# Kernel optimization log

Hardware: AMD Instinct MI355X
Metric: run time of the kernel (lower is better)

## Reference

```python
import jax, jax.numpy as jnp
import numpy as np

H = 32      # num_attention_heads
HD = 64     # head_dim
MD = 64     # qk_mqa_dim (rope dim)
EPS = 1e-6
SCALING = (HD + MD) ** -0.5
NEG = -1e9


def rms_norm(x, w):
    var = jnp.mean(jnp.square(x), axis=-1, keepdims=True)
    return x * jax.lax.rsqrt(var + EPS) * w


def rotate_half(x):
    x1, x2 = jnp.split(x, 2, axis=-1)
    return jnp.concatenate([-x2, x1], axis=-1)


def apply_rope(x, cos, sin):
    return x * cos + rotate_half(x) * sin


def setup_inputs() -> dict:
    key = jax.random.key(0)
    ks = jax.random.split(key, 6)
    B, S, D = 1, 2048, 2048
    QR, KVR = 1024, 896
    hidden_states = jax.random.normal(ks[0], (B, S, D), jnp.float32)
    # real rotary tables for the MD-dim rope subspace
    inv_freq = 1.0 / (10000.0 ** (np.arange(0, MD, 2, dtype=np.float32) / MD))
    freqs = np.arange(S, dtype=np.float32)[:, None] * inv_freq[None, :]
    emb = np.concatenate([freqs, freqs], axis=-1)  # [S, MD]
    cos = jnp.asarray(np.cos(emb), jnp.float32)
    sin = jnp.asarray(np.sin(emb), jnp.float32)
    s = 0.02
    Wqa = jax.random.normal(ks[1], (QR, D), jnp.float32) * s
    q_ln_w = jnp.ones((QR,), jnp.float32)
    Wqb = jax.random.normal(ks[2], (H * (HD + MD), QR), jnp.float32) * s
    Wkva = jax.random.normal(ks[3], (KVR + MD, D), jnp.float32) * s
    kv_ln_w = jnp.ones((KVR,), jnp.float32)
    Wkvb = jax.random.normal(ks[4], (2 * H * HD, KVR), jnp.float32) * s
    Wo = jax.random.normal(ks[5], (D, H * HD), jnp.float32) * s
    return {"hidden_states": hidden_states, "cos": cos, "sin": sin,
            "Wqa": Wqa, "q_ln_w": q_ln_w, "Wqb": Wqb,
            "Wkva": Wkva, "kv_ln_w": kv_ln_w, "Wkvb": Wkvb, "Wo": Wo}


def reference(hidden_states, cos, sin, Wqa, q_ln_w, Wqb, Wkva, kv_ln_w, Wkvb, Wo):
    B, S, D = hidden_states.shape
    KVR = kv_ln_w.shape[0]
    # Q: LoRA down -> RMSNorm -> up (weights pre-absorbed with rope split)
    q = rms_norm(hidden_states @ Wqa.T, q_ln_w) @ Wqb.T      # [B,S,H*(HD+MD)]
    q = q.reshape(B, S, H, HD + MD).transpose(0, 2, 1, 3)     # [B,H,S,HD+MD]
    q_nope, q_rope = q[..., :HD], q[..., HD:]
    # KV: shared compressed latent + MQA rope key
    ckv = hidden_states @ Wkva.T                               # [B,S,KVR+MD]
    kv_nope, k_rope = ckv[..., :KVR], ckv[..., KVR:]
    kv_nope = rms_norm(kv_nope, kv_ln_w)
    q_rope = apply_rope(q_rope, cos[None, None], sin[None, None])
    k_rope = apply_rope(k_rope[:, None], cos[None, None], sin[None, None])  # [B,1,S,MD]
    # up-project latent to per-head K_nope and V (interleaved per head)
    kv = (kv_nope @ Wkvb.T).reshape(B, S, H, 2 * HD).transpose(0, 2, 1, 3)  # [B,H,S,2*HD]
    k_nope, value = kv[..., :HD], kv[..., HD:]
    key_states = jnp.concatenate(
        [k_nope, jnp.broadcast_to(k_rope, (B, H, S, MD))], axis=-1)  # repeat_kv of rope part
    query_states = jnp.concatenate([q_nope, q_rope], axis=-1)        # [B,H,S,HD+MD]
    # causal SDPA with scaling = (head_dim + qk_mqa_dim)^-0.5
    scores = jnp.einsum('bhqd,bhkd->bhqk', query_states, key_states) * SCALING
    causal = jnp.tril(jnp.ones((S, S), bool))
    scores = jnp.where(causal[None, None], scores, NEG)
    probs = jax.nn.softmax(scores, axis=-1)
    out = jnp.einsum('bhqk,bhkd->bhqd', probs, value)                # [B,H,S,HD]
    out = out.transpose(0, 2, 1, 3).reshape(B, S, H * HD)
    return out @ Wo.T
```

## Files before the change

kernel.cpp:

```cpp
#include <hip/hip_runtime.h>
#include <stdint.h>

typedef unsigned short u16;
typedef __attribute__((ext_vector_type(4))) float f32x4;
typedef __attribute__((ext_vector_type(4))) unsigned short u16x4;
typedef __attribute__((ext_vector_type(8))) unsigned short u16x8;
typedef __attribute__((ext_vector_type(8))) short s16x8;
typedef __attribute__((ext_vector_type(4))) short s16x4;
typedef __attribute__((ext_vector_type(2))) unsigned int u32x2;

#define DEVI static __device__ __forceinline__

#define VMCNT(n) asm volatile("s_waitcnt vmcnt(" #n ")" ::: "memory")
#define SBAR() __builtin_amdgcn_s_barrier()
#define SCHED0() __builtin_amdgcn_sched_barrier(0)

DEVI u16 f2b(float f) {
  union { float f; unsigned u; } v; v.f = f;
  unsigned r = v.u + 0x7fffu + ((v.u >> 16) & 1u);
  return (u16)(r >> 16);
}
DEVI float b2f(u16 b) {
  union { unsigned u; float f; } v; v.u = ((unsigned)b) << 16;
  return v.f;
}

DEVI void gload_lds16(const void* gptr, void* lptr) {
  typedef const __attribute__((address_space(1))) unsigned gq;
  typedef __attribute__((address_space(3))) unsigned lq;
  __builtin_amdgcn_global_load_lds((gq*)(uintptr_t)gptr,
                                   (lq*)(uint32_t)(uintptr_t)lptr, 16, 0, 0);
}

DEVI unsigned cvtpk(float a, float b) {
  unsigned d;
  asm("v_cvt_pk_bf16_f32 %0, %1, %2" : "=v"(d) : "v"(a), "v"(b));
  return d;
}
DEVI f32x4 mfma16(s16x4 a, s16x4 b, f32x4 c) {
  f32x4 d;
  asm("v_mfma_f32_16x16x16_bf16 %0, %1, %2, %3" : "=v"(d) : "v"(a), "v"(b), "v"(c));
  return d;
}
DEVI float exp2a(float x) {
  float d;
  asm("v_exp_f32 %0, %1" : "=v"(d) : "v"(x));
  return d;
}

__global__ __launch_bounds__(256) void cvt_all(
    const float* __restrict__ X, const float* __restrict__ Wqa,
    const float* __restrict__ Wkva, const float* __restrict__ Wqb,
    const float* __restrict__ Wkvb, const float* __restrict__ Wo,
    u16* __restrict__ Xb, u16* __restrict__ W1, u16* __restrict__ Wqbb,
    u16* __restrict__ Wkvbb, u16* __restrict__ Wob) {
  int i = blockIdx.x * 256 + threadIdx.x;
  const int stride = gridDim.x * 256;
  for (; i < 5079040; i += stride) {
    const float* s; u16* d; int j;
    if (i < 1572864) {
      if (i < 1048576) { s = X; d = Xb; j = i; }
      else             { s = Wqa; d = W1; j = i - 1048576; }
    } else if (i < 3112960) {
      if (i < 2064384) { s = Wkva; d = W1 + 1024 * 2048; j = i - 1572864; }
      else             { s = Wqb; d = Wqbb; j = i - 2064384; }
    } else {
      if (i < 4030464) { s = Wkvb; d = Wkvbb; j = i - 3112960; }
      else             { s = Wo; d = Wob; j = i - 4030464; }
    }
    f32x4 v = *(const f32x4*)(s + (size_t)j * 4);
    u16x4 o;
    o[0] = f2b(v[0]); o[1] = f2b(v[1]); o[2] = f2b(v[2]); o[3] = f2b(v[3]);
    *(u16x4*)(d + (size_t)j * 4) = o;
  }
}

#define GEMM_STAGE(AP, BP, KK, k0, buf)                                        \
  {                                                                            \
    _Pragma("unroll") for (int p = 0; p < 4; ++p) {                            \
      const int c = tid + p * 256;                                             \
      const int row = c >> 3, j = c & 7;                                       \
      gload_lds16(AP + (size_t)(m0 + row) * (KK) + (k0) + ((j ^ (row & 7)) * 8), \
                  &As[buf][c * 8]);                                            \
    }                                                                          \
    _Pragma("unroll") for (int p = 0; p < 4; ++p) {                            \
      const int c = tid + p * 256;                                             \
      const int row = c >> 3, j = c & 7;                                       \
      gload_lds16(BP + (size_t)(n0 + row) * (KK) + (k0) + ((j ^ (row & 7)) * 8), \
                  &Bs[buf][c * 8]);                                            \
    }                                                                          \
  }

#define GEMM_COMPUTE(cur)                                                      \
  _Pragma("unroll") for (int kk = 0; kk < 64; kk += 32) {                      \
    s16x8 af[4], bfr[4];                                                       \
    _Pragma("unroll") for (int i = 0; i < 4; ++i) {                            \
      const int rA = wm * 64 + i * 16 + c15;                                   \
      af[i] = *(const s16x8*)((const char*)&As[cur][0] + rA * 128 +            \
                              (((kk + g * 8) * 2) ^ ((rA & 7) << 4)));         \
    }                                                                          \
    _Pragma("unroll") for (int i = 0; i < 4; ++i) {                            \
      const int rB = wn * 64 + i * 16 + c15;                                   \
      bfr[i] = *(const s16x8*)((const char*)&Bs[cur][0] + rB * 128 +           \
                               (((kk + g * 8) * 2) ^ ((rB & 7) << 4)));        \
    }                                                                          \
    _Pragma("unroll") for (int i = 0; i < 4; ++i)                              \
      _Pragma("unroll") for (int j = 0; j < 4; ++j)                            \
        acc[i][j] = __builtin_amdgcn_mfma_f32_16x16x32_bf16(af[i], bfr[j],     \
                                                            acc[i][j], 0, 0, 0); \
  }

#define GEMM_PROLOG                                                            \
  const int tid = threadIdx.x;                                                 \
  const int lane = tid & 63, w = tid >> 6;                                     \
  const int wm = w >> 1, wn = w & 1;                                           \
  const int c15 = lane & 15, g = lane >> 4;                                    \
  const int m0 = blockIdx.y * 128, n0 = blockIdx.x * 128;                      \
  f32x4 acc[4][4] = {};

#define GEMM_LOOP(AP, BP, KK)                                                  \
  GEMM_STAGE(AP, BP, KK, 0, 0);                                                \
  const int nk = (KK) >> 6;                                                    \
  for (int kt = 0; kt < nk; ++kt) {                                            \
    const int cur = kt & 1;                                                    \
    if (kt + 1 < nk) {                                                         \
      GEMM_STAGE(AP, BP, KK, (kt + 1) << 6, cur ^ 1);                          \
      VMCNT(8);                                                                \
    } else {                                                                   \
      VMCNT(0);                                                                \
    }                                                                          \
    SBAR(); SCHED0();                                                          \
    GEMM_COMPUTE(cur);                                                         \
    SBAR(); SCHED0();                                                          \
  }

#define GEMM_LOOP3(AP, BP, KK)                                                 \
  GEMM_STAGE(AP, BP, KK, 0, 0);                                                \
  GEMM_STAGE(AP, BP, KK, 64, 1);                                               \
  const int nk = (KK) >> 6;                                                    \
  int bufc = 0;                                                                \
  for (int kt = 0; kt < nk; ++kt) {                                            \
    const int nxt = (bufc + 2 >= 3) ? bufc - 1 : bufc + 2;                     \
    if (kt + 2 < nk) {                                                         \
      GEMM_STAGE(AP, BP, KK, (kt + 2) << 6, nxt);                              \
      VMCNT(16);                                                               \
    } else if (kt + 1 < nk) {                                                  \
      VMCNT(8);                                                                \
    } else {                                                                   \
      VMCNT(0);                                                                \
    }                                                                          \
    SBAR(); SCHED0();                                                          \
    GEMM_COMPUTE(bufc);                                                        \
    SBAR(); SCHED0();                                                          \
    bufc = (bufc + 1 == 3) ? 0 : bufc + 1;                                     \
  }

template <int OUT_BF16>
__global__ __launch_bounds__(256) void gemm_out(const u16* __restrict__ A,
                                                const u16* __restrict__ B,
                                                void* __restrict__ Cv,
                                                int M, int N, int K) {
  __shared__ __align__(16) u16 As[3][128 * 64];
  __shared__ __align__(16) u16 Bs[3][128 * 64];
  GEMM_PROLOG
  GEMM_LOOP3(A, B, K)
#pragma unroll
  for (int i = 0; i < 4; ++i)
#pragma unroll
    for (int j = 0; j < 4; ++j) {
      const int mr = m0 + wm * 64 + i * 16 + g * 4;
      const int nc = n0 + wn * 64 + j * 16 + c15;
#pragma unroll
      for (int r = 0; r < 4; ++r) {
        if (OUT_BF16)
          ((u16*)Cv)[(size_t)(mr + r) * N + nc] = f2b(acc[i][j][r]);
        else
          ((float*)Cv)[(size_t)(mr + r) * N + nc] = acc[i][j][r];
      }
    }
}

__global__ __launch_bounds__(256) void gemm2_fused(
    const u16* __restrict__ qn, const u16* __restrict__ Wqbb,
    const u16* __restrict__ kvn, const u16* __restrict__ Wkvbb,
    u16* __restrict__ qraw, char* __restrict__ KbB, char* __restrict__ VtB) {
  __shared__ __align__(16) u16 As[2][128 * 64];
  __shared__ __align__(16) u16 Bs[2][128 * 64];
  const int z = blockIdx.z;
  const u16* A = z ? kvn : qn;
  const u16* B = z ? Wkvbb : Wqbb;
  const int K = z ? 896 : 1024;
  GEMM_PROLOG
  GEMM_LOOP(A, B, K)

  if (z == 0) {
#pragma unroll
    for (int i = 0; i < 4; ++i)
#pragma unroll
      for (int j = 0; j < 4; ++j) {
        const int mr = m0 + wm * 64 + i * 16 + g * 4;
        const int nc = n0 + wn * 64 + j * 16 + c15;
#pragma unroll
        for (int r = 0; r < 4; ++r)
          qraw[(size_t)(mr + r) * 4096 + nc] = f2b(acc[i][j][r]);
      }
  } else {
    const int h = n0 >> 7;
#pragma unroll
    for (int i = 0; i < 4; ++i)
#pragma unroll
      for (int j = 0; j < 4; ++j) {
        const int mr = m0 + wm * 64 + i * 16 + g * 4;
        if (wn == 0) {
          const int d = j * 16 + c15;
#pragma unroll
          for (int r = 0; r < 4; ++r) {
            const int s = mr + r;
            *(u16*)(KbB + ((size_t)(h * 2048 + s) << 8) +
                    ((2 * d) ^ ((s & 7) << 4))) = f2b(acc[i][j][r]);
          }
        } else {
          const int d = j * 16 + c15;
          u16x4 o;
#pragma unroll
          for (int r = 0; r < 4; ++r) o[r] = f2b(acc[i][j][r]);
          *(u16x4*)(VtB + ((size_t)(h * 64 + d) << 12) +
                    ((2 * mr) ^ ((d & 7) << 4))) = o;
        }
      }
  }
}

DEVI float block_sum(float v, float* sbuf, int tid) {
#pragma unroll
  for (int o = 32; o; o >>= 1) v += __shfl_xor(v, o, 64);
  __syncthreads();
  if ((tid & 63) == 0) sbuf[tid >> 6] = v;
  __syncthreads();
  return sbuf[0] + sbuf[1] + sbuf[2] + sbuf[3];
}

__global__ __launch_bounds__(256) void norm_rope(const u16* __restrict__ C1b,
    const float* __restrict__ qw, const float* __restrict__ kw,
    const float* __restrict__ cosb, const float* __restrict__ sinb,
    u16* __restrict__ qn, u16* __restrict__ kvn, char* __restrict__ KbB) {
  __shared__ float sbuf[4];
  __shared__ __align__(16) u16 rv[64];
  const int s = blockIdx.x, tid = threadIdx.x;
  const u16* row = C1b + (size_t)s * 2048;

  u16x4 qv4 = *(const u16x4*)(row + tid * 4);
  float q0 = b2f(qv4[0]), q1 = b2f(qv4[1]), q2 = b2f(qv4[2]), q3 = b2f(qv4[3]);
  float ss = q0*q0 + q1*q1 + q2*q2 + q3*q3;
  ss = block_sum(ss, sbuf, tid);
  const float scale = rsqrtf(ss * (1.f / 1024.f) + 1e-6f);
  {
    f32x4 wv = *(const f32x4*)(qw + tid * 4);
    u16x4 o;
    o[0] = f2b(q0 * scale * wv[0]); o[1] = f2b(q1 * scale * wv[1]);
    o[2] = f2b(q2 * scale * wv[2]); o[3] = f2b(q3 * scale * wv[3]);
    *(u16x4*)(qn + (size_t)s * 1024 + tid * 4) = o;
  }

  float ss2 = 0.f;
  float k0 = 0, k1 = 0, k2 = 0, k3 = 0;
  if (tid < 224) {
    u16x4 kv4 = *(const u16x4*)(row + 1024 + tid * 4);
    k0 = b2f(kv4[0]); k1 = b2f(kv4[1]); k2 = b2f(kv4[2]); k3 = b2f(kv4[3]);
    ss2 = k0*k0 + k1*k1 + k2*k2 + k3*k3;
  }
  ss2 = block_sum(ss2, sbuf, tid);
  const float sc2 = rsqrtf(ss2 * (1.f / 896.f) + 1e-6f);
  if (tid < 224) {
    f32x4 wv = *(const f32x4*)(kw + tid * 4);
    u16x4 o;
    o[0] = f2b(k0 * sc2 * wv[0]); o[1] = f2b(k1 * sc2 * wv[1]);
    o[2] = f2b(k2 * sc2 * wv[2]); o[3] = f2b(k3 * sc2 * wv[3]);
    *(u16x4*)(kvn + (size_t)s * 896 + tid * 4) = o;
  }

  if (tid < 64) {
    const int d = tid;
    const float x = b2f(row[1920 + d]);
    const float part = b2f(row[1920 + (d < 32 ? d + 32 : d - 32)]);
    const float cv = cosb[s * 64 + d], sv = sinb[s * 64 + d];
    rv[d] = f2b(d < 32 ? (x * cv - part * sv) : (x * cv + part * sv));
  }
  __syncthreads();
  {
    const int h = tid >> 3, c8 = tid & 7;
    const u16x8 v = *(const u16x8*)&rv[c8 * 8];
    *(u16x8*)(KbB + ((size_t)(h * 2048 + s) << 8) +
              ((128 + c8 * 16) ^ ((s & 7) << 4))) = v;
  }
}

__global__ __launch_bounds__(256) void attn_fwd(
    const u16* __restrict__ Qb, const u16* __restrict__ Kb,
    const u16* __restrict__ Vt, const float* __restrict__ cosb,
    const float* __restrict__ sinb, u16* __restrict__ attn) {
  __shared__ __align__(16) u16 Klds[2][64 * 128];
  __shared__ __align__(16) u16 Vlds[2][64 * 64];
  const int tid = threadIdx.x;
  const int lane = tid & 63, w = tid >> 6;
  const int c15 = lane & 15, g = lane >> 4;
  const int orig = blockIdx.x;
  const int xcd = orig & 7, l = orig >> 3;
  const int h = xcd * 4 + (l & 3);
  const int x = l >> 2;
  const int qb = (x < 8) ? (15 - x) : (x - 8);
  const int wmin = qb * 128 + w * 32;
  const int wmax = wmin + 31;
  const char* KbHB = (const char*)Kb + ((size_t)h << 19);
  const char* VtHB = (const char*)Vt + ((size_t)h << 18);
  const float SC2 = 0.12753860478587782f;

  s16x8 qf[2][4];
#pragma unroll
  for (int qa = 0; qa < 2; ++qa) {
    const int qrow = wmin + qa * 16 + c15;
    const u16* qp = Qb + (size_t)qrow * 4096 + h * 128;
    u16x8 x0 = *(const u16x8*)(qp + g * 8);
    u16x8 x1 = *(const u16x8*)(qp + 32 + g * 8);
    u16x8 x2 = *(const u16x8*)(qp + 64 + g * 8);
    u16x8 x3 = *(const u16x8*)(qp + 96 + g * 8);
    const float* cb = cosb + (size_t)qrow * 64 + g * 8;
    const float* sb = sinb + (size_t)qrow * 64 + g * 8;
#pragma unroll
    for (int i = 0; i < 8; ++i) {
      qf[qa][0][i] = (short)f2b(b2f(x0[i]) * SC2);
      qf[qa][1][i] = (short)f2b(b2f(x1[i]) * SC2);
      const float f2 = b2f(x2[i]), f3 = b2f(x3[i]);
      qf[qa][2][i] = (short)f2b((f2 * cb[i] - f3 * sb[i]) * SC2);
      qf[qa][3][i] = (short)f2b((f3 * cb[32 + i] + f2 * sb[32 + i]) * SC2);
    }
  }

  const int nt = 2 * qb + 2;
  auto STAGE = [&](int t, int buf) {
    const int kv0 = t << 6;
#pragma unroll
    for (int p = 0; p < 4; ++p) {
      const int c = tid + p * 256;
      gload_lds16(KbHB + ((size_t)(kv0 + (c >> 4)) << 8) + (c & 15) * 16,
                  (char*)Klds[buf] + c * 16);
    }
#pragma unroll
    for (int p = 0; p < 2; ++p) {
      const int c = tid + p * 256;
      gload_lds16(VtHB + ((size_t)(c >> 3) << 12) + 2 * kv0 + (c & 7) * 16,
                  (char*)Vlds[buf] + c * 16);
    }
  };

  f32x4 acc[2][4] = {};
  float m[2] = {-1e9f, -1e9f}, ssum[2] = {0.f, 0.f};

  STAGE(0, 0);

  for (int t = 0; t < nt; ++t) {
    const int cur = t & 1;
    const int kv0 = t << 6;
    if (t + 1 < nt) {
      STAGE(t + 1, cur ^ 1);
      VMCNT(6);
    } else {
      VMCNT(0);
    }
    SBAR();
    SCHED0();

    if (kv0 <= wmax) {
      const u16* Kc = Klds[cur];
      const u16* Vc = Vlds[cur];

      float pv[2][4][4];
      __builtin_amdgcn_s_setprio(1);
#pragma unroll
      for (int kvh = 0; kvh < 4; ++kvh) {
        s16x8 kf[4];
        const int rb = (kvh * 16 + c15) * 256;
#pragma unroll
        for (int d0 = 0; d0 < 4; ++d0)
          kf[d0] = *(const s16x8*)((const char*)Kc + rb +
                                   ((d0 * 64 + g * 16) ^ ((c15 & 7) << 4)));
#pragma unroll
        for (int qa = 0; qa < 2; ++qa) {
          f32x4 s4 = {};
#pragma unroll
          for (int d0 = 0; d0 < 4; ++d0)
            s4 = __builtin_amdgcn_mfma_f32_16x16x32_bf16(kf[d0], qf[qa][d0], s4, 0, 0, 0);
          pv[qa][kvh][0] = s4[0]; pv[qa][kvh][1] = s4[1];
          pv[qa][kvh][2] = s4[2]; pv[qa][kvh][3] = s4[3];
        }
      }
      __builtin_amdgcn_s_setprio(0);

      if (kv0 + 63 > wmin) {
#pragma unroll
        for (int qa = 0; qa < 2; ++qa) {
          const int qrow = wmin + qa * 16 + c15;
#pragma unroll
          for (int kvh = 0; kvh < 4; ++kvh)
#pragma unroll
            for (int r = 0; r < 4; ++r) {
              const int kv = kv0 + kvh * 16 + g * 4 + r;
              if (kv > qrow) pv[qa][kvh][r] = -1e9f;
            }
        }
      }

      s16x4 pB[2][4];
#pragma unroll
      for (int qa = 0; qa < 2; ++qa) {
        float pm = -1e9f;
#pragma unroll
        for (int kvh = 0; kvh < 4; ++kvh)
#pragma unroll
          for (int r = 0; r < 4; ++r) pm = fmaxf(pm, pv[qa][kvh][r]);
        pm = fmaxf(pm, __shfl_xor(pm, 16, 64));
        pm = fmaxf(pm, __shfl_xor(pm, 32, 64));
        if (!__all(pm - m[qa] <= 8.f)) {
          const float mnew = fmaxf(m[qa], pm);
          const float alpha = exp2a(m[qa] - mnew);
          ssum[qa] *= alpha;
#pragma unroll
          for (int dt = 0; dt < 4; ++dt) acc[qa][dt] *= alpha;
          m[qa] = mnew;
        }
#pragma unroll
        for (int kvh = 0; kvh < 4; ++kvh)
#pragma unroll
          for (int r = 0; r < 4; ++r) {
            const float p = exp2a(pv[qa][kvh][r] - m[qa]);
            pv[qa][kvh][r] = p;
            ssum[qa] += p;
          }
#pragma unroll
        for (int ks = 0; ks < 4; ++ks) {
          u32x2 pw;
          pw[0] = cvtpk(pv[qa][ks][0], pv[qa][ks][1]);
          pw[1] = cvtpk(pv[qa][ks][2], pv[qa][ks][3]);
          pB[qa][ks] = __builtin_bit_cast(s16x4, pw);
        }
      }

      __builtin_amdgcn_s_setprio(1);
#pragma unroll
      for (int dt = 0; dt < 4; ++dt) {
        const int rb2 = (dt * 16 + c15) * 128;
#pragma unroll
        for (int ks = 0; ks < 4; ++ks) {
          s16x4 vf = *(const s16x4*)((const char*)Vc + rb2 +
                                     ((ks * 32 + g * 8) ^ ((c15 & 7) << 4)));
          acc[0][dt] = mfma16(vf, pB[0][ks], acc[0][dt]);
          acc[1][dt] = mfma16(vf, pB[1][ks], acc[1][dt]);
        }
      }
      __builtin_amdgcn_s_setprio(0);
    }
    SBAR();
    SCHED0();
  }

#pragma unroll
  for (int qa = 0; qa < 2; ++qa) {
    float sv = ssum[qa];
    sv += __shfl_xor(sv, 16, 64);
    sv += __shfl_xor(sv, 32, 64);
    const float inv = 1.f / sv;
    const int qrow = wmin + qa * 16 + c15;
#pragma unroll
    for (int dt = 0; dt < 4; ++dt) {
      u16x4 o;
#pragma unroll
      for (int r = 0; r < 4; ++r) o[r] = f2b(acc[qa][dt][r] * inv);
      *(u16x4*)(attn + (size_t)qrow * 2048 + h * 64 + dt * 16 + g * 4) = o;
    }
  }
}

extern "C" void kernel_launch(void* const* d_in, const int* in_sizes, int n_in,
                              void* d_out, int out_size, void* d_ws, size_t ws_size,
                              hipStream_t stream) {
  const float* X    = (const float*)d_in[0];
  const float* cosb = (const float*)d_in[1];
  const float* sinb = (const float*)d_in[2];
  const float* Wqa  = (const float*)d_in[3];
  const float* qlnw = (const float*)d_in[4];
  const float* Wqb  = (const float*)d_in[5];
  const float* Wkva = (const float*)d_in[6];
  const float* klnw = (const float*)d_in[7];
  const float* Wkvb = (const float*)d_in[8];
  const float* Wo   = (const float*)d_in[9];
  float* out = (float*)d_out;
  char* ws = (char*)d_ws;

  u16*   Xb     = (u16*)(ws + 0);
  u16*   W1     = (u16*)(ws + 8388608);
  u16*   C1b    = (u16*)(ws + 16777216);
  u16*   qn     = (u16*)(ws + 33554432);
  u16*   kvn    = (u16*)(ws + 37748736);
  u16*   Wqbb   = (u16*)(ws + 41943040);
  u16*   Wkvbb  = (u16*)(ws + 50331648);
  u16*   qraw_b = (u16*)(ws + 0);
  u16*   Kb     = (u16*)(ws + 58720256);
  u16*   VtG    = (u16*)(ws + 75497472);
  u16*   attnb  = (u16*)(ws + 83886080);
  u16*   Wob    = (u16*)(ws + 92274688);

  cvt_all<<<2048, 256, 0, stream>>>(X, Wqa, Wkva, Wqb, Wkvb, Wo,
                                    Xb, W1, Wqbb, Wkvbb, Wob);

  gemm_out<1><<<dim3(16, 16), 256, 0, stream>>>(Xb, W1, C1b, 2048, 2048, 2048);

  norm_rope<<<2048, 256, 0, stream>>>(C1b, qlnw, klnw, cosb, sinb, qn, kvn, (char*)Kb);

  gemm2_fused<<<dim3(32, 16, 2), 256, 0, stream>>>(qn, Wqbb, kvn, Wkvbb,
                                                   qraw_b, (char*)Kb, (char*)VtG);

  attn_fwd<<<512, 256, 0, stream>>>(qraw_b, Kb, VtG, cosb, sinb, attnb);

  gemm_out<0><<<dim3(16, 16), 256, 0, stream>>>(attnb, Wob, out, 2048, 2048, 2048);
}
```

Baseline: 172.8 us.

## Pair causal query blocks per 512-thread workgroup with 128-row KV tiles

```diff
diff --git a/kernel.cpp b/kernel.cpp
--- a/kernel.cpp
+++ b/kernel.cpp
@@ -295,12 +295,12 @@
   }
 }
 
-__global__ __launch_bounds__(256) void attn_fwd(
+__global__ __launch_bounds__(512) void attn_fwd(
     const u16* __restrict__ Qb, const u16* __restrict__ Kb,
     const u16* __restrict__ Vt, const float* __restrict__ cosb,
     const float* __restrict__ sinb, u16* __restrict__ attn) {
-  __shared__ __align__(16) u16 Klds[2][64 * 128];
-  __shared__ __align__(16) u16 Vlds[2][64 * 64];
+  __shared__ __align__(16) u16 Klds[2][128 * 128];
+  __shared__ __align__(16) u16 Vlds[2][64 * 128];
   const int tid = threadIdx.x;
   const int lane = tid & 63, w = tid >> 6;
   const int c15 = lane & 15, g = lane >> 4;
@@ -308,8 +308,9 @@
   const int xcd = orig & 7, l = orig >> 3;
   const int h = xcd * 4 + (l & 3);
   const int x = l >> 2;
-  const int qb = (x < 8) ? (15 - x) : (x - 8);
-  const int wmin = qb * 128 + w * 32;
+  const int grp = w >> 2, w4 = w & 3;
+  const int j = grp ? x : 15 - x;
+  const int wmin = j * 128 + w4 * 32;
   const int wmax = wmin + 31;
   const char* KbHB = (const char*)Kb + ((size_t)h << 19);
   const char* VtHB = (const char*)Vt + ((size_t)h << 18);
@@ -336,19 +337,19 @@
     }
   }
 
-  const int nt = 2 * qb + 2;
+  const int nt = 16 - x;
   auto STAGE = [&](int t, int buf) {
-    const int kv0 = t << 6;
+    const int kv0 = t << 7;
 #pragma unroll
     for (int p = 0; p < 4; ++p) {
-      const int c = tid + p * 256;
+      const int c = tid + p * 512;
       gload_lds16(KbHB + ((size_t)(kv0 + (c >> 4)) << 8) + (c & 15) * 16,
                   (char*)Klds[buf] + c * 16);
     }
 #pragma unroll
     for (int p = 0; p < 2; ++p) {
-      const int c = tid + p * 256;
-      gload_lds16(VtHB + ((size_t)(c >> 3) << 12) + 2 * kv0 + (c & 7) * 16,
+      const int c = tid + p * 512;
+      gload_lds16(VtHB + ((size_t)(c >> 4) << 12) + 2 * kv0 + (c & 15) * 16,
                   (char*)Vlds[buf] + c * 16);
     }
   };
@@ -360,7 +361,7 @@
 
   for (int t = 0; t < nt; ++t) {
     const int cur = t & 1;
-    const int kv0 = t << 6;
+    const int kv0 = t << 7;
     if (t + 1 < nt) {
       STAGE(t + 1, cur ^ 1);
       VMCNT(6);
@@ -373,17 +374,17 @@
     if (kv0 <= wmax) {
       const u16* Kc = Klds[cur];
       const u16* Vc = Vlds[cur];
-
-      float pv[2][4][4];
+      const int swz = (c15 & 7) << 4;
+
+      float pv[2][8][4];
       __builtin_amdgcn_s_setprio(1);
 #pragma unroll
-      for (int kvh = 0; kvh < 4; ++kvh) {
+      for (int kvh = 0; kvh < 8; ++kvh) {
         s16x8 kf[4];
         const int rb = (kvh * 16 + c15) * 256;
 #pragma unroll
         for (int d0 = 0; d0 < 4; ++d0)
-          kf[d0] = *(const s16x8*)((const char*)Kc + rb +
-                                   ((d0 * 64 + g * 16) ^ ((c15 & 7) << 4)));
+          kf[d0] = *(const s16x8*)((const char*)Kc + rb + ((d0 * 64 + g * 16) ^ swz));
 #pragma unroll
         for (int qa = 0; qa < 2; ++qa) {
           f32x4 s4 = {};
@@ -396,26 +397,22 @@
       }
       __builtin_amdgcn_s_setprio(0);
 
-      if (kv0 + 63 > wmin) {
-#pragma unroll
-        for (int qa = 0; qa < 2; ++qa) {
+      const bool diag = (kv0 + 127 > wmin);
+#pragma unroll
+      for (int qa = 0; qa < 2; ++qa) {
+        if (diag) {
           const int qrow = wmin + qa * 16 + c15;
 #pragma unroll
-          for (int kvh = 0; kvh < 4; ++kvh)
+          for (int kvh = 0; kvh < 8; ++kvh)
 #pragma unroll
             for (int r = 0; r < 4; ++r) {
               const int kv = kv0 + kvh * 16 + g * 4 + r;
               if (kv > qrow) pv[qa][kvh][r] = -1e9f;
             }
         }
-      }
-
-      s16x4 pB[2][4];
-#pragma unroll
-      for (int qa = 0; qa < 2; ++qa) {
         float pm = -1e9f;
 #pragma unroll
-        for (int kvh = 0; kvh < 4; ++kvh)
+        for (int kvh = 0; kvh < 8; ++kvh)
 #pragma unroll
           for (int r = 0; r < 4; ++r) pm = fmaxf(pm, pv[qa][kvh][r]);
         pm = fmaxf(pm, __shfl_xor(pm, 16, 64));
@@ -428,36 +425,32 @@
           for (int dt = 0; dt < 4; ++dt) acc[qa][dt] *= alpha;
           m[qa] = mnew;
         }
-#pragma unroll
-        for (int kvh = 0; kvh < 4; ++kvh)
+        s16x4 pB[8];
+#pragma unroll
+        for (int kvh = 0; kvh < 8; ++kvh) {
 #pragma unroll
           for (int r = 0; r < 4; ++r) {
             const float p = exp2a(pv[qa][kvh][r] - m[qa]);
             pv[qa][kvh][r] = p;
             ssum[qa] += p;
           }
-#pragma unroll
-        for (int ks = 0; ks < 4; ++ks) {
           u32x2 pw;
-          pw[0] = cvtpk(pv[qa][ks][0], pv[qa][ks][1]);
-          pw[1] = cvtpk(pv[qa][ks][2], pv[qa][ks][3]);
-          pB[qa][ks] = __builtin_bit_cast(s16x4, pw);
+          pw[0] = cvtpk(pv[qa][kvh][0], pv[qa][kvh][1]);
+          pw[1] = cvtpk(pv[qa][kvh][2], pv[qa][kvh][3]);
+          pB[kvh] = __builtin_bit_cast(s16x4, pw);
         }
+        __builtin_amdgcn_s_setprio(1);
+#pragma unroll
+        for (int dt = 0; dt < 4; ++dt) {
+          const int rb2 = (dt * 16 + c15) * 256;
+#pragma unroll
+          for (int ks = 0; ks < 8; ++ks) {
+            s16x4 vf = *(const s16x4*)((const char*)Vc + rb2 + ((ks * 32 + g * 8) ^ swz));
+            acc[qa][dt] = mfma16(vf, pB[ks], acc[qa][dt]);
+          }
+        }
+        __builtin_amdgcn_s_setprio(0);
       }
-
-      __builtin_amdgcn_s_setprio(1);
-#pragma unroll
-      for (int dt = 0; dt < 4; ++dt) {
-        const int rb2 = (dt * 16 + c15) * 128;
-#pragma unroll
-        for (int ks = 0; ks < 4; ++ks) {
-          s16x4 vf = *(const s16x4*)((const char*)Vc + rb2 +
-                                     ((ks * 32 + g * 8) ^ ((c15 & 7) << 4)));
-          acc[0][dt] = mfma16(vf, pB[0][ks], acc[0][dt]);
-          acc[1][dt] = mfma16(vf, pB[1][ks], acc[1][dt]);
-        }
-      }
-      __builtin_amdgcn_s_setprio(0);
     }
     SBAR();
     SCHED0();
@@ -519,7 +512,7 @@
   gemm2_fused<<<dim3(32, 16, 2), 256, 0, stream>>>(qn, Wqbb, kvn, Wkvbb,
                                                    qraw_b, (char*)Kb, (char*)VtG);
 
-  attn_fwd<<<512, 256, 0, stream>>>(qraw_b, Kb, VtG, cosb, sinb, attnb);
+  attn_fwd<<<256, 512, 0, stream>>>(qraw_b, Kb, VtG, cosb, sinb, attnb);
 
   gemm_out<0><<<dim3(16, 16), 256, 0, stream>>>(attnb, Wob, out, 2048, 2048, 2048);
 }
```

Result: no change. 176.1 us (+1.9%).

## Split attention KV range in two halves and merge with log-sum-exp combine

Applied to the files above, without the earlier changes.

```diff
diff --git a/kernel.cpp b/kernel.cpp
--- a/kernel.cpp
+++ b/kernel.cpp
@@ -298,7 +298,8 @@
 __global__ __launch_bounds__(256) void attn_fwd(
     const u16* __restrict__ Qb, const u16* __restrict__ Kb,
     const u16* __restrict__ Vt, const float* __restrict__ cosb,
-    const float* __restrict__ sinb, u16* __restrict__ attn) {
+    const float* __restrict__ sinb, u16* __restrict__ O1, u16* __restrict__ O2,
+    float* __restrict__ L1, float* __restrict__ L2) {
   __shared__ __align__(16) u16 Klds[2][64 * 128];
   __shared__ __align__(16) u16 Vlds[2][64 * 64];
   const int tid = threadIdx.x;
@@ -307,8 +308,12 @@
   const int orig = blockIdx.x;
   const int xcd = orig & 7, l = orig >> 3;
   const int h = xcd * 4 + (l & 3);
-  const int x = l >> 2;
-  const int qb = (x < 8) ? (15 - x) : (x - 8);
+  const int rem = l >> 2;
+  const int half = rem & 1;
+  const int qb = 15 - (rem >> 1);
+  const int kvbase = half ? 64 * (qb + 1) : 0;
+  u16* Oh = half ? O2 : O1;
+  float* Lh = half ? L2 : L1;
   const int wmin = qb * 128 + w * 32;
   const int wmax = wmin + 31;
   const char* KbHB = (const char*)Kb + ((size_t)h << 19);
@@ -336,19 +341,19 @@
     }
   }
 
-  const int nt = 2 * qb + 2;
+  const int nt = qb + 1;
   auto STAGE = [&](int t, int buf) {
-    const int kv0 = t << 6;
+    const int kv0g = kvbase + (t << 6);
 #pragma unroll
     for (int p = 0; p < 4; ++p) {
       const int c = tid + p * 256;
-      gload_lds16(KbHB + ((size_t)(kv0 + (c >> 4)) << 8) + (c & 15) * 16,
+      gload_lds16(KbHB + ((size_t)(kv0g + (c >> 4)) << 8) + (c & 15) * 16,
                   (char*)Klds[buf] + c * 16);
     }
 #pragma unroll
     for (int p = 0; p < 2; ++p) {
       const int c = tid + p * 256;
-      gload_lds16(VtHB + ((size_t)(c >> 3) << 12) + 2 * kv0 + (c & 7) * 16,
+      gload_lds16(VtHB + ((size_t)(c >> 3) << 12) + 2 * kv0g + (c & 7) * 16,
                   (char*)Vlds[buf] + c * 16);
     }
   };
@@ -360,7 +365,7 @@
 
   for (int t = 0; t < nt; ++t) {
     const int cur = t & 1;
-    const int kv0 = t << 6;
+    const int kv0g = kvbase + (t << 6);
     if (t + 1 < nt) {
       STAGE(t + 1, cur ^ 1);
       VMCNT(6);
@@ -370,7 +375,7 @@
     SBAR();
     SCHED0();
 
-    if (kv0 <= wmax) {
+    if (kv0g <= wmax) {
       const u16* Kc = Klds[cur];
       const u16* Vc = Vlds[cur];
 
@@ -396,7 +401,7 @@
       }
       __builtin_amdgcn_s_setprio(0);
 
-      if (kv0 + 63 > wmin) {
+      if (kv0g + 63 > wmin) {
 #pragma unroll
         for (int qa = 0; qa < 2; ++qa) {
           const int qrow = wmin + qa * 16 + c15;
@@ -404,7 +409,7 @@
           for (int kvh = 0; kvh < 4; ++kvh)
 #pragma unroll
             for (int r = 0; r < 4; ++r) {
-              const int kv = kv0 + kvh * 16 + g * 4 + r;
+              const int kv = kv0g + kvh * 16 + g * 4 + r;
               if (kv > qrow) pv[qa][kvh][r] = -1e9f;
             }
         }
@@ -468,16 +473,38 @@
     float sv = ssum[qa];
     sv += __shfl_xor(sv, 16, 64);
     sv += __shfl_xor(sv, 32, 64);
-    const float inv = 1.f / sv;
+    const float inv = (sv > 0.f) ? 1.f / sv : 0.f;
     const int qrow = wmin + qa * 16 + c15;
 #pragma unroll
     for (int dt = 0; dt < 4; ++dt) {
       u16x4 o;
 #pragma unroll
       for (int r = 0; r < 4; ++r) o[r] = f2b(acc[qa][dt][r] * inv);
-      *(u16x4*)(attn + (size_t)qrow * 2048 + h * 64 + dt * 16 + g * 4) = o;
-    }
-  }
+      *(u16x4*)(Oh + (size_t)qrow * 2048 + h * 64 + dt * 16 + g * 4) = o;
+    }
+    if (g == 0)
+      Lh[qrow * 32 + h] = (sv > 0.f) ? m[qa] + __log2f(sv) : -3.0e38f;
+  }
+}
+
+__global__ __launch_bounds__(256) void attn_combine(
+    const u16* __restrict__ O1, const u16* __restrict__ O2,
+    const float* __restrict__ L1, const float* __restrict__ L2,
+    u16* __restrict__ attnb) {
+  const int idx = blockIdx.x * 256 + threadIdx.x;
+  const int base = idx * 8;
+  const int qh = base >> 6;
+  const float l1 = L1[qh], l2 = L2[qh];
+  const float Lm = fmaxf(l1, l2);
+  const float w1 = exp2a(l1 - Lm), w2 = exp2a(l2 - Lm);
+  const float inv = 1.f / (w1 + w2);
+  u16x8 a = *(const u16x8*)(O1 + base);
+  u16x8 b = *(const u16x8*)(O2 + base);
+  u16x8 o;
+#pragma unroll
+  for (int i = 0; i < 8; ++i)
+    o[i] = f2b((b2f(a[i]) * w1 + b2f(b[i]) * w2) * inv);
+  *(u16x8*)(attnb + base) = o;
 }
 
 extern "C" void kernel_launch(void* const* d_in, const int* in_sizes, int n_in,
@@ -508,6 +535,10 @@
   u16*   VtG    = (u16*)(ws + 75497472);
   u16*   attnb  = (u16*)(ws + 83886080);
   u16*   Wob    = (u16*)(ws + 92274688);
+  float* L1buf  = (float*)(ws + 33554432);
+  float* L2buf  = (float*)(ws + 33554432 + 262144);
+  u16*   O1buf  = (u16*)(ws + 41943040);
+  u16*   O2buf  = (u16*)(ws + 50331648);
 
   cvt_all<<<2048, 256, 0, stream>>>(X, Wqa, Wkva, Wqb, Wkvb, Wo,
                                     Xb, W1, Wqbb, Wkvbb, Wob);
@@ -519,7 +550,10 @@
   gemm2_fused<<<dim3(32, 16, 2), 256, 0, stream>>>(qn, Wqbb, kvn, Wkvbb,
                                                    qraw_b, (char*)Kb, (char*)VtG);
 
-  attn_fwd<<<512, 256, 0, stream>>>(qraw_b, Kb, VtG, cosb, sinb, attnb);
+  attn_fwd<<<1024, 256, 0, stream>>>(qraw_b, Kb, VtG, cosb, sinb,
+                                     O1buf, O2buf, L1buf, L2buf);
+
+  attn_combine<<<2048, 256, 0, stream>>>(O1buf, O2buf, L1buf, L2buf, attnb);
 
   gemm_out<0><<<dim3(16, 16), 256, 0, stream>>>(attnb, Wob, out, 2048, 2048, 2048);
 }
```

After: 175.9 us. About the same (+1.7%).

## Drop LDS staging in attention; load K/V fragments directly from global

Applied to the files above, without the earlier changes.

```diff
diff --git a/kernel.cpp b/kernel.cpp
--- a/kernel.cpp
+++ b/kernel.cpp
@@ -216,16 +216,14 @@
 #pragma unroll
           for (int r = 0; r < 4; ++r) {
             const int s = mr + r;
-            *(u16*)(KbB + ((size_t)(h * 2048 + s) << 8) +
-                    ((2 * d) ^ ((s & 7) << 4))) = f2b(acc[i][j][r]);
+            *(u16*)(KbB + ((size_t)(h * 2048 + s) << 8) + 2 * d) = f2b(acc[i][j][r]);
           }
         } else {
           const int d = j * 16 + c15;
           u16x4 o;
 #pragma unroll
           for (int r = 0; r < 4; ++r) o[r] = f2b(acc[i][j][r]);
-          *(u16x4*)(VtB + ((size_t)(h * 64 + d) << 12) +
-                    ((2 * mr) ^ ((d & 7) << 4))) = o;
+          *(u16x4*)(VtB + ((size_t)(h * 64 + d) << 12) + 2 * mr) = o;
         }
       }
   }
@@ -290,27 +288,24 @@
   {
     const int h = tid >> 3, c8 = tid & 7;
     const u16x8 v = *(const u16x8*)&rv[c8 * 8];
-    *(u16x8*)(KbB + ((size_t)(h * 2048 + s) << 8) +
-              ((128 + c8 * 16) ^ ((s & 7) << 4))) = v;
-  }
-}
-
-__global__ __launch_bounds__(256) void attn_fwd(
+    *(u16x8*)(KbB + ((size_t)(h * 2048 + s) << 8) + 128 + c8 * 16) = v;
+  }
+}
+
+__global__ __launch_bounds__(128) void attn_fwd(
     const u16* __restrict__ Qb, const u16* __restrict__ Kb,
     const u16* __restrict__ Vt, const float* __restrict__ cosb,
-    const float* __restrict__ sinb, u16* __restrict__ attn) {
-  __shared__ __align__(16) u16 Klds[2][64 * 128];
-  __shared__ __align__(16) u16 Vlds[2][64 * 64];
+    const float* __restrict__ sinb, u16* __restrict__ attnb) {
   const int tid = threadIdx.x;
   const int lane = tid & 63, w = tid >> 6;
   const int c15 = lane & 15, g = lane >> 4;
   const int orig = blockIdx.x;
   const int xcd = orig & 7, l = orig >> 3;
   const int h = xcd * 4 + (l & 3);
-  const int x = l >> 2;
-  const int qb = (x < 8) ? (15 - x) : (x - 8);
-  const int wmin = qb * 128 + w * 32;
-  const int wmax = wmin + 31;
+  const int i4 = l >> 2;
+  const int qt = (i4 < 8) ? 31 - i4 : (i4 < 16) ? i4 - 8
+               : (i4 < 24) ? 39 - i4 : i4 - 16;
+  const int wmin = qt * 64 + w * 32;
   const char* KbHB = (const char*)Kb + ((size_t)h << 19);
   const char* VtHB = (const char*)Vt + ((size_t)h << 18);
   const float SC2 = 0.12753860478587782f;
@@ -336,131 +331,105 @@
     }
   }
 
-  const int nt = 2 * qb + 2;
-  auto STAGE = [&](int t, int buf) {
-    const int kv0 = t << 6;
-#pragma unroll
-    for (int p = 0; p < 4; ++p) {
-      const int c = tid + p * 256;
-      gload_lds16(KbHB + ((size_t)(kv0 + (c >> 4)) << 8) + (c & 15) * 16,
-                  (char*)Klds[buf] + c * 16);
-    }
-#pragma unroll
-    for (int p = 0; p < 2; ++p) {
-      const int c = tid + p * 256;
-      gload_lds16(VtHB + ((size_t)(c >> 3) << 12) + 2 * kv0 + (c & 7) * 16,
-                  (char*)Vlds[buf] + c * 16);
-    }
-  };
-
+  const int nt = qt + 1;
   f32x4 acc[2][4] = {};
   float m[2] = {-1e9f, -1e9f}, ssum[2] = {0.f, 0.f};
 
-  STAGE(0, 0);
-
   for (int t = 0; t < nt; ++t) {
-    const int cur = t & 1;
     const int kv0 = t << 6;
-    if (t + 1 < nt) {
-      STAGE(t + 1, cur ^ 1);
-      VMCNT(6);
-    } else {
-      VMCNT(0);
-    }
-    SBAR();
-    SCHED0();
-
-    if (kv0 <= wmax) {
-      const u16* Kc = Klds[cur];
-      const u16* Vc = Vlds[cur];
-
-      float pv[2][4][4];
-      __builtin_amdgcn_s_setprio(1);
-#pragma unroll
-      for (int kvh = 0; kvh < 4; ++kvh) {
-        s16x8 kf[4];
-        const int rb = (kvh * 16 + c15) * 256;
+
+    s16x8 kf[4][4];
+#pragma unroll
+    for (int kvh = 0; kvh < 4; ++kvh) {
+      const char* rp = KbHB + (size_t)(kv0 + kvh * 16 + c15) * 256 + g * 16;
+#pragma unroll
+      for (int d0 = 0; d0 < 4; ++d0)
+        kf[kvh][d0] = *(const s16x8*)(rp + d0 * 64);
+    }
+    s16x4 vf[4][4];
+#pragma unroll
+    for (int dt = 0; dt < 4; ++dt) {
+      const char* vp = VtHB + (size_t)(dt * 16 + c15) * 4096 + 2 * (kv0 + g * 4);
+#pragma unroll
+      for (int ks = 0; ks < 4; ++ks)
+        vf[dt][ks] = *(const s16x4*)(vp + ks * 32);
+    }
+
+    float pv[2][4][4];
+    __builtin_amdgcn_s_setprio(1);
+#pragma unroll
+    for (int kvh = 0; kvh < 4; ++kvh) {
+#pragma unroll
+      for (int qa = 0; qa < 2; ++qa) {
+        f32x4 s4 = {};
 #pragma unroll
         for (int d0 = 0; d0 < 4; ++d0)
-          kf[d0] = *(const s16x8*)((const char*)Kc + rb +
-                                   ((d0 * 64 + g * 16) ^ ((c15 & 7) << 4)));
-#pragma unroll
-        for (int qa = 0; qa < 2; ++qa) {
-          f32x4 s4 = {};
-#pragma unroll
-          for (int d0 = 0; d0 < 4; ++d0)
-            s4 = __builtin_amdgcn_mfma_f32_16x16x32_bf16(kf[d0], qf[qa][d0], s4, 0, 0, 0);
-          pv[qa][kvh][0] = s4[0]; pv[qa][kvh][1] = s4[1];
-          pv[qa][kvh][2] = s4[2]; pv[qa][kvh][3] = s4[3];
+          s4 = __builtin_amdgcn_mfma_f32_16x16x32_bf16(kf[kvh][d0], qf[qa][d0], s4, 0, 0, 0);
+        pv[qa][kvh][0] = s4[0]; pv[qa][kvh][1] = s4[1];
+        pv[qa][kvh][2] = s4[2]; pv[qa][kvh][3] = s4[3];
+      }
+    }
+    __builtin_amdgcn_s_setprio(0);
+
+    if (kv0 + 63 > wmin) {
+#pragma unroll
+      for (int qa = 0; qa < 2; ++qa) {
+        const int qrow = wmin + qa * 16 + c15;
+#pragma unroll
+        for (int kvh = 0; kvh < 4; ++kvh)
+#pragma unroll
+          for (int r = 0; r < 4; ++r) {
+            const int kv = kv0 + kvh * 16 + g * 4 + r;
+            if (kv > qrow) pv[qa][kvh][r] = -1e9f;
+          }
+      }
+    }
+
+    s16x4 pB[2][4];
+#pragma unroll
+    for (int qa = 0; qa < 2; ++qa) {
+      float pml = -1e9f;
+#pragma unroll
+      for (int kvh = 0; kvh < 4; ++kvh)
+#pragma unroll
+        for (int r = 0; r < 4; ++r) pml = fmaxf(pml, pv[qa][kvh][r]);
+      if (!__all(pml - m[qa] <= 8.f)) {
+        float pm = fmaxf(pml, __shfl_xor(pml, 16, 64));
+        pm = fmaxf(pm, __shfl_xor(pm, 32, 64));
+        const float mnew = fmaxf(m[qa], pm);
+        const float alpha = exp2a(m[qa] - mnew);
+        ssum[qa] *= alpha;
+#pragma unroll
+        for (int dt = 0; dt < 4; ++dt) acc[qa][dt] *= alpha;
+        m[qa] = mnew;
+      }
+#pragma unroll
+      for (int kvh = 0; kvh < 4; ++kvh)
+#pragma unroll
+        for (int r = 0; r < 4; ++r) {
+          const float p = exp2a(pv[qa][kvh][r] - m[qa]);
+          pv[qa][kvh][r] = p;
+          ssum[qa] += p;
         }
-      }
-      __builtin_amdgcn_s_setprio(0);
-
-      if (kv0 + 63 > wmin) {
-#pragma unroll
-        for (int qa = 0; qa < 2; ++qa) {
-          const int qrow = wmin + qa * 16 + c15;
-#pragma unroll
-          for (int kvh = 0; kvh < 4; ++kvh)
-#pragma unroll
-            for (int r = 0; r < 4; ++r) {
-              const int kv = kv0 + kvh * 16 + g * 4 + r;
-              if (kv > qrow) pv[qa][kvh][r] = -1e9f;
-            }
-        }
-      }
-
-      s16x4 pB[2][4];
-#pragma unroll
-      for (int qa = 0; qa < 2; ++qa) {
-        float pm = -1e9f;
-#pragma unroll
-        for (int kvh = 0; kvh < 4; ++kvh)
-#pragma unroll
-          for (int r = 0; r < 4; ++r) pm = fmaxf(pm, pv[qa][kvh][r]);
-        pm = fmaxf(pm, __shfl_xor(pm, 16, 64));
-        pm = fmaxf(pm, __shfl_xor(pm, 32, 64));
-        if (!__all(pm - m[qa] <= 8.f)) {
-          const float mnew = fmaxf(m[qa], pm);
-          const float alpha = exp2a(m[qa] - mnew);
-          ssum[qa] *= alpha;
-#pragma unroll
-          for (int dt = 0; dt < 4; ++dt) acc[qa][dt] *= alpha;
-          m[qa] = mnew;
-        }
-#pragma unroll
-        for (int kvh = 0; kvh < 4; ++kvh)
-#pragma unroll
-          for (int r = 0; r < 4; ++r) {
-            const float p = exp2a(pv[qa][kvh][r] - m[qa]);
-            pv[qa][kvh][r] = p;
-            ssum[qa] += p;
-          }
-#pragma unroll
-        for (int ks = 0; ks < 4; ++ks) {
-          u32x2 pw;
-          pw[0] = cvtpk(pv[qa][ks][0], pv[qa][ks][1]);
-          pw[1] = cvtpk(pv[qa][ks][2], pv[qa][ks][3]);
-          pB[qa][ks] = __builtin_bit_cast(s16x4, pw);
-        }
-      }
-
-      __builtin_amdgcn_s_setprio(1);
-#pragma unroll
-      for (int dt = 0; dt < 4; ++dt) {
-        const int rb2 = (dt * 16 + c15) * 128;
-#pragma unroll
-        for (int ks = 0; ks < 4; ++ks) {
-          s16x4 vf = *(const s16x4*)((const char*)Vc + rb2 +
-                                     ((ks * 32 + g * 8) ^ ((c15 & 7) << 4)));
-          acc[0][dt] = mfma16(vf, pB[0][ks], acc[0][dt]);
-          acc[1][dt] = mfma16(vf, pB[1][ks], acc[1][dt]);
-        }
-      }
-      __builtin_amdgcn_s_setprio(0);
-    }
-    SBAR();
-    SCHED0();
+#pragma unroll
+      for (int ks = 0; ks < 4; ++ks) {
+        u32x2 pw;
+        pw[0] = cvtpk(pv[qa][ks][0], pv[qa][ks][1]);
+        pw[1] = cvtpk(pv[qa][ks][2], pv[qa][ks][3]);
+        pB[qa][ks] = __builtin_bit_cast(s16x4, pw);
+      }
+    }
+
+    __builtin_amdgcn_s_setprio(1);
+#pragma unroll
+    for (int dt = 0; dt < 4; ++dt) {
+#pragma unroll
+      for (int ks = 0; ks < 4; ++ks) {
+        acc[0][dt] = mfma16(vf[dt][ks], pB[0][ks], acc[0][dt]);
+        acc[1][dt] = mfma16(vf[dt][ks], pB[1][ks], acc[1][dt]);
+      }
+    }
+    __builtin_amdgcn_s_setprio(0);
   }
 
 #pragma unroll
@@ -475,7 +444,7 @@
       u16x4 o;
 #pragma unroll
       for (int r = 0; r < 4; ++r) o[r] = f2b(acc[qa][dt][r] * inv);
-      *(u16x4*)(attn + (size_t)qrow * 2048 + h * 64 + dt * 16 + g * 4) = o;
+      *(u16x4*)(attnb + (size_t)qrow * 2048 + h * 64 + dt * 16 + g * 4) = o;
     }
   }
 }
@@ -519,7 +488,7 @@
   gemm2_fused<<<dim3(32, 16, 2), 256, 0, stream>>>(qn, Wqbb, kvn, Wkvbb,
                                                    qraw_b, (char*)Kb, (char*)VtG);
 
-  attn_fwd<<<512, 256, 0, stream>>>(qraw_b, Kb, VtG, cosb, sinb, attnb);
+  attn_fwd<<<1024, 128, 0, stream>>>(qraw_b, Kb, VtG, cosb, sinb, attnb);
 
   gemm_out<0><<<dim3(16, 16), 256, 0, stream>>>(attnb, Wob, out, 2048, 2048, 2048);
 }
```

New measurement: 237.9 us. +37.7%, slower.
